# Kernel optimization log

Measured on AMD Instinct MI355X. Metric: run time of the kernel, lower is better.

The kernel has to match this reference:

```python
import jax, jax.numpy as jnp
import numpy as np

N_NODES = 100000
N_EDGES = 1600000
D_IN = 128
D_HID = 128
D_OUT = 128


def setup_inputs() -> dict:
    key = jax.random.key(0)
    ks = jax.random.split(key, 9)
    x = jax.random.normal(ks[0], (N_NODES, D_IN), dtype=jnp.float32)
    src = jax.random.randint(ks[1], (N_EDGES,), 0, N_NODES, dtype=jnp.int32)
    dst = jax.random.randint(ks[2], (N_EDGES,), 0, N_NODES, dtype=jnp.int32)
    def lin(k, fan_in, fan_out):
        bound = 1.0 / np.sqrt(fan_in)
        return jax.random.uniform(k, (fan_out, fan_in), jnp.float32, -bound, bound)
    W_self1 = lin(ks[3], D_IN, D_HID)
    W_neigh1 = lin(ks[4], D_IN, D_HID)
    b1 = jnp.zeros((D_HID,), jnp.float32)
    W_self2 = lin(ks[5], D_HID, D_OUT)
    W_neigh2 = lin(ks[6], D_HID, D_OUT)
    b2 = jnp.zeros((D_OUT,), jnp.float32)
    return {"x": x, "src": src, "dst": dst,
            "W_self1": W_self1, "W_neigh1": W_neigh1, "b1": b1,
            "W_self2": W_self2, "W_neigh2": W_neigh2, "b2": b2}


def _sage_conv(x, src, dst, W_self, W_neigh, b):
    # mean aggregation over in-neighbors (DGL SAGEConv 'mean')
    msg_sum = jax.ops.segment_sum(x[src], dst, num_segments=N_NODES)  # [N, d]
    deg = jax.ops.segment_sum(jnp.ones((src.shape[0],), x.dtype), dst,
                              num_segments=N_NODES)
    h_neigh = msg_sum / jnp.maximum(deg, 1.0)[:, None]
    return x @ W_self.T + h_neigh @ W_neigh.T + b


def reference(x, src, dst, W_self1, W_neigh1, b1, W_self2, W_neigh2, b2):
    h = _sage_conv(x, src, dst, W_self1, W_neigh1, b1)
    h = _sage_conv(h, src, dst, W_self2, W_neigh2, b2)
    # F.normalize(h, p=2, dim=1), eps=1e-12
    norm = jnp.linalg.norm(h, axis=1, keepdims=True)
    return h / jnp.maximum(norm, 1e-12)
```

## Files before the change

### kernel.cpp

```cpp
#include <hip/hip_runtime.h>
#include <math.h>

#define DIM 128
#define CAP 8192
#define BSHIFT 8
#define MAXNB 512

typedef __attribute__((ext_vector_type(8))) short bf16x8;
typedef __attribute__((ext_vector_type(8))) unsigned short us8;
typedef __attribute__((ext_vector_type(4))) float f32x4;

__device__ __forceinline__ unsigned short f2bf_rne(float f) {
    unsigned int u = __float_as_uint(f);
    unsigned int r = (u + 0x7FFFu + ((u >> 16) & 1u)) >> 16;
    return (unsigned short)r;
}
__device__ __forceinline__ float bf2f(unsigned short h) {
    return __uint_as_float(((unsigned int)h) << 16);
}

__global__ void k_zero_int(int* __restrict__ p, int n) {
    int i = blockIdx.x * blockDim.x + threadIdx.x;
    if (i < n) p[i] = 0;
}

__global__ __launch_bounds__(256) void k_xcvt(const float* __restrict__ in,
                                              unsigned short* __restrict__ outb,
                                              int n4) {
    int i = blockIdx.x * 256 + threadIdx.x;
    int stride = gridDim.x * 256;
    for (; i < n4; i += stride) {
        float4 v = *(const float4*)(in + (size_t)i * 4);
        ushort4 o;
        o.x = f2bf_rne(v.x);
        o.y = f2bf_rne(v.y);
        o.z = f2bf_rne(v.z);
        o.w = f2bf_rne(v.w);
        *(ushort4*)(outb + (size_t)i * 4) = o;
    }
}

__global__ __launch_bounds__(256) void k_wcvt(const float* __restrict__ Ws1,
                                              const float* __restrict__ Wn1,
                                              const float* __restrict__ Ws2,
                                              const float* __restrict__ Wn2,
                                              unsigned short* __restrict__ Wh,
                                              unsigned short* __restrict__ Wl) {
    int i = blockIdx.x * 256 + threadIdx.x;
    int l = i >> 15;
    int rem = i & 32767;
    int n = rem >> 8;
    int k = rem & 255;
    const float* W = (k < 128) ? (l ? Ws2 : Ws1) : (l ? Wn2 : Wn1);
    float f = W[n * 128 + (k & 127)];
    unsigned short h = f2bf_rne(f);
    Wh[i] = h;
    Wl[i] = f2bf_rne(f - bf2f(h));
}

__global__ __launch_bounds__(256) void k_bucket(const int* __restrict__ src,
                                                const int* __restrict__ dst,
                                                int* __restrict__ bcur,
                                                unsigned int* __restrict__ tmpe,
                                                int E, int NB, int chunk) {
    __shared__ int hist[MAXNB];
    __shared__ int cur[MAXNB];
    int t = threadIdx.x;
    int begE = blockIdx.x * chunk;
    int endE = begE + chunk;
    if (endE > E) endE = E;

    hist[t] = 0;
    hist[t + 256] = 0;
    __syncthreads();

    for (int e = begE + t; e < endE; e += 256) {
        atomicAdd(&hist[dst[e] >> BSHIFT], 1);
    }
    __syncthreads();

    if (t < NB)  cur[t]  = atomicAdd(&bcur[t], hist[t]);
    int t2 = t + 256;
    if (t2 < NB) cur[t2] = atomicAdd(&bcur[t2], hist[t2]);
    __syncthreads();

    for (int e = begE + t; e < endE; e += 256) {
        int s = src[e];
        int d = dst[e];
        int b = d >> BSHIFT;
        int p = atomicAdd(&cur[b], 1);
        if (p < CAP) tmpe[(size_t)b * CAP + p] = (unsigned int)s | ((unsigned int)(d & 255) << 17);
    }
}

__global__ __launch_bounds__(256) void k_scatter(unsigned int* __restrict__ tmpe,
                                                 const int* __restrict__ bcur,
                                                 int* __restrict__ rs,
                                                 int* __restrict__ cnt,
                                                 int N) {
    __shared__ unsigned int se[CAP];
    __shared__ int hist[256];
    __shared__ int sh[256];
    __shared__ int cur[256];
    int b = blockIdx.x;
    int t = threadIdx.x;
    size_t base = (size_t)b * CAP;
    int m = bcur[b];
    if (m > CAP) m = CAP;
    for (int i = t; i < m; i += 256) se[i] = tmpe[base + i];
    hist[t] = 0;
    __syncthreads();
    for (int i = t; i < m; i += 256) atomicAdd(&hist[se[i] >> 17], 1);
    __syncthreads();
    int v = hist[t];
    sh[t] = v;
    __syncthreads();
    int run = v;
    for (int off = 1; off < 256; off <<= 1) {
        int y = (t >= off) ? sh[t - off] : 0;
        __syncthreads();
        run += y;
        sh[t] = run;
        __syncthreads();
    }
    int excl = run - v;
    int node = (b << BSHIFT) + t;
    if (node < N) {
        rs[node] = (int)base + excl;
        cnt[node] = v;
    }
    cur[t] = excl;
    __syncthreads();
    for (int i = t; i < m; i += 256) {
        unsigned int pk = se[i];
        int d = pk >> 17;
        int p = atomicAdd(&cur[d], 1);
        tmpe[base + p] = pk & 0x1FFFFu;
    }
}

__global__ __launch_bounds__(256) void k_agg(const unsigned short* __restrict__ in,
                                             const int* __restrict__ rs,
                                             const int* __restrict__ cnt,
                                             const unsigned int* __restrict__ esrc,
                                             float* __restrict__ msg, int N) {
    int w = threadIdx.x >> 6;
    int half = (threadIdx.x >> 5) & 1;
    int l32 = threadIdx.x & 31;
    int node = blockIdx.x * 4 + w;
    if (node >= N) return;
    int beg = rs[node];
    int deg = cnt[node];
    int end = beg + deg;
    int c = l32 * 4;
    float ax = 0.f, ay = 0.f, az = 0.f, aw = 0.f;
    int e = beg + half;
    for (; e + 6 < end; e += 8) {
        int s0 = esrc[e];
        int s1 = esrc[e + 2];
        int s2 = esrc[e + 4];
        int s3 = esrc[e + 6];
        ushort4 u0 = *(const ushort4*)(in + (size_t)s0 * DIM + c);
        ushort4 u1 = *(const ushort4*)(in + (size_t)s1 * DIM + c);
        ushort4 u2 = *(const ushort4*)(in + (size_t)s2 * DIM + c);
        ushort4 u3 = *(const ushort4*)(in + (size_t)s3 * DIM + c);
        ax += (bf2f(u0.x) + bf2f(u1.x)) + (bf2f(u2.x) + bf2f(u3.x));
        ay += (bf2f(u0.y) + bf2f(u1.y)) + (bf2f(u2.y) + bf2f(u3.y));
        az += (bf2f(u0.z) + bf2f(u1.z)) + (bf2f(u2.z) + bf2f(u3.z));
        aw += (bf2f(u0.w) + bf2f(u1.w)) + (bf2f(u2.w) + bf2f(u3.w));
    }
    for (; e + 2 < end; e += 4) {
        int s0 = esrc[e];
        int s1 = esrc[e + 2];
        ushort4 u0 = *(const ushort4*)(in + (size_t)s0 * DIM + c);
        ushort4 u1 = *(const ushort4*)(in + (size_t)s1 * DIM + c);
        ax += bf2f(u0.x) + bf2f(u1.x);
        ay += bf2f(u0.y) + bf2f(u1.y);
        az += bf2f(u0.z) + bf2f(u1.z);
        aw += bf2f(u0.w) + bf2f(u1.w);
    }
    if (e < end) {
        int s0 = esrc[e];
        ushort4 u0 = *(const ushort4*)(in + (size_t)s0 * DIM + c);
        ax += bf2f(u0.x);
        ay += bf2f(u0.y);
        az += bf2f(u0.z);
        aw += bf2f(u0.w);
    }
    ax += __shfl_xor(ax, 32);
    ay += __shfl_xor(ay, 32);
    az += __shfl_xor(az, 32);
    aw += __shfl_xor(aw, 32);
    if (half == 0) {
        float invd = 1.0f / fmaxf((float)deg, 1.0f);
        float4 o;
        o.x = ax * invd;
        o.y = ay * invd;
        o.z = az * invd;
        o.w = aw * invd;
        *(float4*)(msg + (size_t)node * DIM + c) = o;
    }
}

template <bool FUSE_NORM>
__global__ __launch_bounds__(256) void k_gemm(const float* __restrict__ A,
                                              const float* __restrict__ Hn,
                                              const unsigned short* __restrict__ Wh,
                                              const unsigned short* __restrict__ Wl,
                                              const float* __restrict__ bias,
                                              float* __restrict__ out,
                                              unsigned short* __restrict__ outb,
                                              int N, int layer) {
    __shared__ __align__(16) unsigned short Ah[128 * 64];
    __shared__ __align__(16) unsigned short Al[128 * 64];
    __shared__ __align__(16) unsigned short Bh[128 * 64];
    __shared__ __align__(16) unsigned short Bl[128 * 64];
    int tid = threadIdx.x;
    int w = tid >> 6;
    int lane = tid & 63;
    int l4 = lane & 15;
    int g = lane >> 4;
    int m0 = blockIdx.x * 128;
    const unsigned short* WhL = Wh + layer * 128 * 256;
    const unsigned short* WlL = Wl + layer * 128 * 256;

    f32x4 acc[2][8];
#pragma unroll
    for (int rt = 0; rt < 2; ++rt)
#pragma unroll
        for (int ct = 0; ct < 8; ++ct) acc[rt][ct] = (f32x4){0.f, 0.f, 0.f, 0.f};

    for (int kb = 0; kb < 256; kb += 64) {
        const float* srcA = (kb < 128) ? A : Hn;
        int ka = kb & 127;
#pragma unroll
        for (int i = 0; i < 4; ++i) {
            int seg = tid + i * 256;
            int row = seg >> 3, k8 = seg & 7;
            int m = m0 + row;
            float4 v0 = make_float4(0.f, 0.f, 0.f, 0.f);
            float4 v1 = make_float4(0.f, 0.f, 0.f, 0.f);
            if (m < N) {
                const float* p = srcA + (size_t)m * DIM + ka + k8 * 8;
                v0 = *(const float4*)p;
                v1 = *(const float4*)(p + 4);
            }
            float f[8] = {v0.x, v0.y, v0.z, v0.w, v1.x, v1.y, v1.z, v1.w};
            us8 hv, lv;
#pragma unroll
            for (int j = 0; j < 8; ++j) {
                unsigned short h = f2bf_rne(f[j]);
                hv[j] = h;
                lv[j] = f2bf_rne(f[j] - bf2f(h));
            }
            int us = row * 64 + ((k8 ^ (row & 7)) << 3);
            *(us8*)&Ah[us] = hv;
            *(us8*)&Al[us] = lv;
        }
#pragma unroll
        for (int i = 0; i < 4; ++i) {
            int seg = tid + i * 256;
            int n = seg >> 3, k8 = seg & 7;
            int gi = n * 256 + kb + k8 * 8;
            us8 hv = *(const us8*)&WhL[gi];
            us8 lv = *(const us8*)&WlL[gi];
            int us = n * 64 + ((k8 ^ (n & 7)) << 3);
            *(us8*)&Bh[us] = hv;
            *(us8*)&Bl[us] = lv;
        }
        __syncthreads();
#pragma unroll
        for (int ks = 0; ks < 2; ++ks) {
            bf16x8 ah[2], al[2];
#pragma unroll
            for (int rt = 0; rt < 2; ++rt) {
                int row = w * 32 + rt * 16 + l4;
                int us = row * 64 + (((ks * 4 + g) ^ (row & 7)) << 3);
                ah[rt] = *(const bf16x8*)&Ah[us];
                al[rt] = *(const bf16x8*)&Al[us];
            }
#pragma unroll
            for (int ct = 0; ct < 8; ++ct) {
                int n = ct * 16 + l4;
                int us = n * 64 + (((ks * 4 + g) ^ (n & 7)) << 3);
                bf16x8 bh = *(const bf16x8*)&Bh[us];
                bf16x8 bl = *(const bf16x8*)&Bl[us];
#pragma unroll
                for (int rt = 0; rt < 2; ++rt) {
                    acc[rt][ct] = __builtin_amdgcn_mfma_f32_16x16x32_bf16(ah[rt], bh, acc[rt][ct], 0, 0, 0);
                    acc[rt][ct] = __builtin_amdgcn_mfma_f32_16x16x32_bf16(ah[rt], bl, acc[rt][ct], 0, 0, 0);
                    acc[rt][ct] = __builtin_amdgcn_mfma_f32_16x16x32_bf16(al[rt], bh, acc[rt][ct], 0, 0, 0);
                }
            }
        }
        __syncthreads();
    }

    float bv[8];
#pragma unroll
    for (int ct = 0; ct < 8; ++ct) bv[ct] = bias[ct * 16 + l4];
#pragma unroll
    for (int rt = 0; rt < 2; ++rt) {
        int rbase = m0 + w * 32 + rt * 16 + g * 4;
        float vals[8][4];
#pragma unroll
        for (int ct = 0; ct < 8; ++ct)
#pragma unroll
            for (int r = 0; r < 4; ++r) vals[ct][r] = acc[rt][ct][r] + bv[ct];
        if (FUSE_NORM) {
            float ss[4];
#pragma unroll
            for (int r = 0; r < 4; ++r) {
                float s = 0.f;
#pragma unroll
                for (int ct = 0; ct < 8; ++ct) s += vals[ct][r] * vals[ct][r];
                s += __shfl_xor(s, 1);
                s += __shfl_xor(s, 2);
                s += __shfl_xor(s, 4);
                s += __shfl_xor(s, 8);
                ss[r] = s;
            }
#pragma unroll
            for (int r = 0; r < 4; ++r) {
                float sc = 1.0f / fmaxf(sqrtf(ss[r]), 1e-12f);
#pragma unroll
                for (int ct = 0; ct < 8; ++ct) vals[ct][r] *= sc;
            }
        }
#pragma unroll
        for (int r = 0; r < 4; ++r) {
            int m = rbase + r;
            if (m < N) {
#pragma unroll
                for (int ct = 0; ct < 8; ++ct) {
                    out[(size_t)m * DIM + ct * 16 + l4] = vals[ct][r];
                    if (!FUSE_NORM)
                        outb[(size_t)m * DIM + ct * 16 + l4] = f2bf_rne(vals[ct][r]);
                }
            }
        }
    }
}

extern "C" void kernel_launch(void* const* d_in, const int* in_sizes, int n_in,
                              void* d_out, int out_size, void* d_ws, size_t ws_size,
                              hipStream_t stream) {
    const float* x   = (const float*)d_in[0];
    const int*   src = (const int*)d_in[1];
    const int*   dst = (const int*)d_in[2];
    const float* Ws1 = (const float*)d_in[3];
    const float* Wn1 = (const float*)d_in[4];
    const float* b1  = (const float*)d_in[5];
    const float* Ws2 = (const float*)d_in[6];
    const float* Wn2 = (const float*)d_in[7];
    const float* b2  = (const float*)d_in[8];
    float* out = (float*)d_out;

    int N = in_sizes[0] / DIM;
    int E = in_sizes[1];
    int NB = (N + (1 << BSHIFT) - 1) >> BSHIFT;

    char* p = (char*)d_ws;
    size_t off = 0;
    auto carve = [&](size_t bytes) {
        void* r = p + off;
        off = (off + bytes + 255) & ~(size_t)255;
        return r;
    };
    unsigned int* tmpe = (unsigned int*)carve((size_t)NB * CAP * 4);
    int* bcur = (int*)carve((size_t)NB * 4);
    int* rs   = (int*)carve((size_t)N * 4);
    int* cnt  = (int*)carve((size_t)N * 4);
    float* msg = (float*)carve((size_t)N * DIM * 4);
    float* h1  = (float*)carve((size_t)N * DIM * 4);
    unsigned short* xb  = (unsigned short*)carve((size_t)N * DIM * 2);
    unsigned short* h1b = (unsigned short*)carve((size_t)N * DIM * 2);
    unsigned short* Wh = (unsigned short*)carve((size_t)2 * 128 * 256 * 2);
    unsigned short* Wl = (unsigned short*)carve((size_t)2 * 128 * 256 * 2);

    k_wcvt<<<256, 256, 0, stream>>>(Ws1, Wn1, Ws2, Wn2, Wh, Wl);
    k_xcvt<<<2048, 256, 0, stream>>>(x, xb, N * DIM / 4);

    int grid_b = 256;
    int chunk = (E + grid_b - 1) / grid_b;
    k_zero_int<<<(NB + 255) / 256, 256, 0, stream>>>(bcur, NB);
    k_bucket<<<grid_b, 256, 0, stream>>>(src, dst, bcur, tmpe, E, NB, chunk);
    k_scatter<<<NB, 256, 0, stream>>>(tmpe, bcur, rs, cnt, N);

    k_agg<<<(N + 3) / 4, 256, 0, stream>>>(xb, rs, cnt, tmpe, msg, N);
    k_gemm<false><<<(N + 127) / 128, 256, 0, stream>>>(x, msg, Wh, Wl, b1, h1, h1b, N, 0);

    k_agg<<<(N + 3) / 4, 256, 0, stream>>>(h1b, rs, cnt, tmpe, msg, N);
    k_gemm<true><<<(N + 127) / 128, 256, 0, stream>>>(h1, msg, Wh, Wl, b2, out, nullptr, N, 1);
}
```

Baseline: 384.4 us.

## Fuse neighbor aggregation into GEMM kernel, keeping mean messages in LDS

```diff
diff --git a/kernel.cpp b/kernel.cpp
--- a/kernel.cpp
+++ b/kernel.cpp
@@ -139,129 +139,132 @@
     }
 }
 
-__global__ __launch_bounds__(256) void k_agg(const unsigned short* __restrict__ in,
-                                             const int* __restrict__ rs,
-                                             const int* __restrict__ cnt,
-                                             const unsigned int* __restrict__ esrc,
-                                             float* __restrict__ msg, int N) {
-    int w = threadIdx.x >> 6;
-    int half = (threadIdx.x >> 5) & 1;
-    int l32 = threadIdx.x & 31;
-    int node = blockIdx.x * 4 + w;
-    if (node >= N) return;
-    int beg = rs[node];
-    int deg = cnt[node];
-    int end = beg + deg;
-    int c = l32 * 4;
-    float ax = 0.f, ay = 0.f, az = 0.f, aw = 0.f;
-    int e = beg + half;
-    for (; e + 6 < end; e += 8) {
-        int s0 = esrc[e];
-        int s1 = esrc[e + 2];
-        int s2 = esrc[e + 4];
-        int s3 = esrc[e + 6];
-        ushort4 u0 = *(const ushort4*)(in + (size_t)s0 * DIM + c);
-        ushort4 u1 = *(const ushort4*)(in + (size_t)s1 * DIM + c);
-        ushort4 u2 = *(const ushort4*)(in + (size_t)s2 * DIM + c);
-        ushort4 u3 = *(const ushort4*)(in + (size_t)s3 * DIM + c);
-        ax += (bf2f(u0.x) + bf2f(u1.x)) + (bf2f(u2.x) + bf2f(u3.x));
-        ay += (bf2f(u0.y) + bf2f(u1.y)) + (bf2f(u2.y) + bf2f(u3.y));
-        az += (bf2f(u0.z) + bf2f(u1.z)) + (bf2f(u2.z) + bf2f(u3.z));
-        aw += (bf2f(u0.w) + bf2f(u1.w)) + (bf2f(u2.w) + bf2f(u3.w));
-    }
-    for (; e + 2 < end; e += 4) {
-        int s0 = esrc[e];
-        int s1 = esrc[e + 2];
-        ushort4 u0 = *(const ushort4*)(in + (size_t)s0 * DIM + c);
-        ushort4 u1 = *(const ushort4*)(in + (size_t)s1 * DIM + c);
-        ax += bf2f(u0.x) + bf2f(u1.x);
-        ay += bf2f(u0.y) + bf2f(u1.y);
-        az += bf2f(u0.z) + bf2f(u1.z);
-        aw += bf2f(u0.w) + bf2f(u1.w);
-    }
-    if (e < end) {
-        int s0 = esrc[e];
-        ushort4 u0 = *(const ushort4*)(in + (size_t)s0 * DIM + c);
-        ax += bf2f(u0.x);
-        ay += bf2f(u0.y);
-        az += bf2f(u0.z);
-        aw += bf2f(u0.w);
-    }
-    ax += __shfl_xor(ax, 32);
-    ay += __shfl_xor(ay, 32);
-    az += __shfl_xor(az, 32);
-    aw += __shfl_xor(aw, 32);
-    if (half == 0) {
-        float invd = 1.0f / fmaxf((float)deg, 1.0f);
-        float4 o;
-        o.x = ax * invd;
-        o.y = ay * invd;
-        o.z = az * invd;
-        o.w = aw * invd;
-        *(float4*)(msg + (size_t)node * DIM + c) = o;
-    }
-}
-
 template <bool FUSE_NORM>
-__global__ __launch_bounds__(256) void k_gemm(const float* __restrict__ A,
-                                              const float* __restrict__ Hn,
-                                              const unsigned short* __restrict__ Wh,
-                                              const unsigned short* __restrict__ Wl,
-                                              const float* __restrict__ bias,
-                                              float* __restrict__ out,
-                                              unsigned short* __restrict__ outb,
-                                              int N, int layer) {
-    __shared__ __align__(16) unsigned short Ah[128 * 64];
-    __shared__ __align__(16) unsigned short Al[128 * 64];
+__global__ __launch_bounds__(256) void k_fused(const float* __restrict__ Afp,
+                                               const unsigned short* __restrict__ Ab,
+                                               const int* __restrict__ rs,
+                                               const int* __restrict__ cnt,
+                                               const unsigned int* __restrict__ esrc,
+                                               const unsigned short* __restrict__ Wh,
+                                               const unsigned short* __restrict__ Wl,
+                                               const float* __restrict__ bias,
+                                               float* __restrict__ out,
+                                               unsigned short* __restrict__ outb,
+                                               int N, int layer) {
+    __shared__ __align__(16) unsigned short Mh[2 * 64 * 64];
+    __shared__ __align__(16) unsigned short Ml[2 * 64 * 64];
+    __shared__ __align__(16) unsigned short Ah[64 * 64];
+    __shared__ __align__(16) unsigned short Al[64 * 64];
     __shared__ __align__(16) unsigned short Bh[128 * 64];
     __shared__ __align__(16) unsigned short Bl[128 * 64];
     int tid = threadIdx.x;
     int w = tid >> 6;
     int lane = tid & 63;
+    int half = lane >> 5;
+    int l32 = lane & 31;
     int l4 = lane & 15;
     int g = lane >> 4;
-    int m0 = blockIdx.x * 128;
+    int m0 = blockIdx.x * 64;
     const unsigned short* WhL = Wh + layer * 128 * 256;
     const unsigned short* WlL = Wl + layer * 128 * 256;
 
-    f32x4 acc[2][8];
-#pragma unroll
-    for (int rt = 0; rt < 2; ++rt)
-#pragma unroll
-        for (int ct = 0; ct < 8; ++ct) acc[rt][ct] = (f32x4){0.f, 0.f, 0.f, 0.f};
-
-    for (int kb = 0; kb < 256; kb += 64) {
-        const float* srcA = (kb < 128) ? A : Hn;
-        int ka = kb & 127;
-#pragma unroll
-        for (int i = 0; i < 4; ++i) {
-            int seg = tid + i * 256;
-            int row = seg >> 3, k8 = seg & 7;
-            int m = m0 + row;
-            float4 v0 = make_float4(0.f, 0.f, 0.f, 0.f);
-            float4 v1 = make_float4(0.f, 0.f, 0.f, 0.f);
-            if (m < N) {
-                const float* p = srcA + (size_t)m * DIM + ka + k8 * 8;
-                v0 = *(const float4*)p;
-                v1 = *(const float4*)(p + 4);
+    int c = l32 * 4;
+    for (int i = 0; i < 16; ++i) {
+        int row = w * 16 + i;
+        int node = m0 + row;
+        int beg = 0, deg = 0;
+        if (node < N) { beg = rs[node]; deg = cnt[node]; }
+        int end = beg + deg;
+        float ax = 0.f, ay = 0.f, az = 0.f, aw_ = 0.f;
+        int e = beg + half;
+        for (; e + 6 < end; e += 8) {
+            int s0 = esrc[e];
+            int s1 = esrc[e + 2];
+            int s2 = esrc[e + 4];
+            int s3 = esrc[e + 6];
+            ushort4 u0 = *(const ushort4*)(Ab + (size_t)s0 * DIM + c);
+            ushort4 u1 = *(const ushort4*)(Ab + (size_t)s1 * DIM + c);
+            ushort4 u2 = *(const ushort4*)(Ab + (size_t)s2 * DIM + c);
+            ushort4 u3 = *(const ushort4*)(Ab + (size_t)s3 * DIM + c);
+            ax += (bf2f(u0.x) + bf2f(u1.x)) + (bf2f(u2.x) + bf2f(u3.x));
+            ay += (bf2f(u0.y) + bf2f(u1.y)) + (bf2f(u2.y) + bf2f(u3.y));
+            az += (bf2f(u0.z) + bf2f(u1.z)) + (bf2f(u2.z) + bf2f(u3.z));
+            aw_ += (bf2f(u0.w) + bf2f(u1.w)) + (bf2f(u2.w) + bf2f(u3.w));
+        }
+        for (; e + 2 < end; e += 4) {
+            int s0 = esrc[e];
+            int s1 = esrc[e + 2];
+            ushort4 u0 = *(const ushort4*)(Ab + (size_t)s0 * DIM + c);
+            ushort4 u1 = *(const ushort4*)(Ab + (size_t)s1 * DIM + c);
+            ax += bf2f(u0.x) + bf2f(u1.x);
+            ay += bf2f(u0.y) + bf2f(u1.y);
+            az += bf2f(u0.z) + bf2f(u1.z);
+            aw_ += bf2f(u0.w) + bf2f(u1.w);
+        }
+        if (e < end) {
+            int s0 = esrc[e];
+            ushort4 u0 = *(const ushort4*)(Ab + (size_t)s0 * DIM + c);
+            ax += bf2f(u0.x);
+            ay += bf2f(u0.y);
+            az += bf2f(u0.z);
+            aw_ += bf2f(u0.w);
+        }
+        ax += __shfl_xor(ax, 32);
+        ay += __shfl_xor(ay, 32);
+        az += __shfl_xor(az, 32);
+        aw_ += __shfl_xor(aw_, 32);
+        if (half == 0) {
+            float invd = 1.0f / fmaxf((float)deg, 1.0f);
+            float f0 = ax * invd, f1 = ay * invd, f2 = az * invd, f3 = aw_ * invd;
+            ushort4 hv, lv;
+            hv.x = f2bf_rne(f0); lv.x = f2bf_rne(f0 - bf2f(hv.x));
+            hv.y = f2bf_rne(f1); lv.y = f2bf_rne(f1 - bf2f(hv.y));
+            hv.z = f2bf_rne(f2); lv.z = f2bf_rne(f2 - bf2f(hv.z));
+            hv.w = f2bf_rne(f3); lv.w = f2bf_rne(f3 - bf2f(hv.w));
+            int ch = l32 >> 4;
+            int k8 = (l32 >> 1) & 7;
+            int us = ch * 4096 + row * 64 + ((k8 ^ (row & 7)) << 3) + ((l32 & 1) << 2);
+            *(ushort4*)&Mh[us] = hv;
+            *(ushort4*)&Ml[us] = lv;
+        }
+    }
+
+    f32x4 acc[8];
+#pragma unroll
+    for (int ct = 0; ct < 8; ++ct) acc[ct] = (f32x4){0.f, 0.f, 0.f, 0.f};
+
+    for (int chunk = 0; chunk < 4; ++chunk) {
+        if (chunk < 2) {
+#pragma unroll
+            for (int i = 0; i < 2; ++i) {
+                int seg = tid + i * 256;
+                int row = seg >> 3, k8 = seg & 7;
+                int m = m0 + row;
+                float4 v0 = make_float4(0.f, 0.f, 0.f, 0.f);
+                float4 v1 = make_float4(0.f, 0.f, 0.f, 0.f);
+                if (m < N) {
+                    const float* p = Afp + (size_t)m * DIM + chunk * 64 + k8 * 8;
+                    v0 = *(const float4*)p;
+                    v1 = *(const float4*)(p + 4);
+                }
+                float f[8] = {v0.x, v0.y, v0.z, v0.w, v1.x, v1.y, v1.z, v1.w};
+                us8 hv, lv;
+#pragma unroll
+                for (int j = 0; j < 8; ++j) {
+                    unsigned short h = f2bf_rne(f[j]);
+                    hv[j] = h;
+                    lv[j] = f2bf_rne(f[j] - bf2f(h));
+                }
+                int us = row * 64 + ((k8 ^ (row & 7)) << 3);
+                *(us8*)&Ah[us] = hv;
+                *(us8*)&Al[us] = lv;
             }
-            float f[8] = {v0.x, v0.y, v0.z, v0.w, v1.x, v1.y, v1.z, v1.w};
-            us8 hv, lv;
-#pragma unroll
-            for (int j = 0; j < 8; ++j) {
-                unsigned short h = f2bf_rne(f[j]);
-                hv[j] = h;
-                lv[j] = f2bf_rne(f[j] - bf2f(h));
-            }
-            int us = row * 64 + ((k8 ^ (row & 7)) << 3);
-            *(us8*)&Ah[us] = hv;
-            *(us8*)&Al[us] = lv;
         }
 #pragma unroll
         for (int i = 0; i < 4; ++i) {
             int seg = tid + i * 256;
             int n = seg >> 3, k8 = seg & 7;
-            int gi = n * 256 + kb + k8 * 8;
+            int gi = n * 256 + chunk * 64 + k8 * 8;
             us8 hv = *(const us8*)&WhL[gi];
             us8 lv = *(const us8*)&WlL[gi];
             int us = n * 64 + ((k8 ^ (n & 7)) << 3);
@@ -269,28 +272,29 @@
             *(us8*)&Bl[us] = lv;
         }
         __syncthreads();
+        int arow = w * 16 + l4;
 #pragma unroll
         for (int ks = 0; ks < 2; ++ks) {
-            bf16x8 ah[2], al[2];
-#pragma unroll
-            for (int rt = 0; rt < 2; ++rt) {
-                int row = w * 32 + rt * 16 + l4;
-                int us = row * 64 + (((ks * 4 + g) ^ (row & 7)) << 3);
-                ah[rt] = *(const bf16x8*)&Ah[us];
-                al[rt] = *(const bf16x8*)&Al[us];
+            int kidx = ks * 4 + g;
+            bf16x8 ah, al;
+            if (chunk < 2) {
+                int us = arow * 64 + ((kidx ^ (arow & 7)) << 3);
+                ah = *(const bf16x8*)&Ah[us];
+                al = *(const bf16x8*)&Al[us];
+            } else {
+                int us = (chunk - 2) * 4096 + arow * 64 + ((kidx ^ (arow & 7)) << 3);
+                ah = *(const bf16x8*)&Mh[us];
+                al = *(const bf16x8*)&Ml[us];
             }
 #pragma unroll
             for (int ct = 0; ct < 8; ++ct) {
                 int n = ct * 16 + l4;
-                int us = n * 64 + (((ks * 4 + g) ^ (n & 7)) << 3);
+                int us = n * 64 + ((kidx ^ (n & 7)) << 3);
                 bf16x8 bh = *(const bf16x8*)&Bh[us];
                 bf16x8 bl = *(const bf16x8*)&Bl[us];
-#pragma unroll
-                for (int rt = 0; rt < 2; ++rt) {
-                    acc[rt][ct] = __builtin_amdgcn_mfma_f32_16x16x32_bf16(ah[rt], bh, acc[rt][ct], 0, 0, 0);
-                    acc[rt][ct] = __builtin_amdgcn_mfma_f32_16x16x32_bf16(ah[rt], bl, acc[rt][ct], 0, 0, 0);
-                    acc[rt][ct] = __builtin_amdgcn_mfma_f32_16x16x32_bf16(al[rt], bh, acc[rt][ct], 0, 0, 0);
-                }
+                acc[ct] = __builtin_amdgcn_mfma_f32_16x16x32_bf16(ah, bh, acc[ct], 0, 0, 0);
+                acc[ct] = __builtin_amdgcn_mfma_f32_16x16x32_bf16(ah, bl, acc[ct], 0, 0, 0);
+                acc[ct] = __builtin_amdgcn_mfma_f32_16x16x32_bf16(al, bh, acc[ct], 0, 0, 0);
             }
         }
         __syncthreads();
@@ -299,44 +303,41 @@
     float bv[8];
 #pragma unroll
     for (int ct = 0; ct < 8; ++ct) bv[ct] = bias[ct * 16 + l4];
-#pragma unroll
-    for (int rt = 0; rt < 2; ++rt) {
-        int rbase = m0 + w * 32 + rt * 16 + g * 4;
-        float vals[8][4];
-#pragma unroll
-        for (int ct = 0; ct < 8; ++ct)
-#pragma unroll
-            for (int r = 0; r < 4; ++r) vals[ct][r] = acc[rt][ct][r] + bv[ct];
-        if (FUSE_NORM) {
-            float ss[4];
-#pragma unroll
-            for (int r = 0; r < 4; ++r) {
-                float s = 0.f;
-#pragma unroll
-                for (int ct = 0; ct < 8; ++ct) s += vals[ct][r] * vals[ct][r];
-                s += __shfl_xor(s, 1);
-                s += __shfl_xor(s, 2);
-                s += __shfl_xor(s, 4);
-                s += __shfl_xor(s, 8);
-                ss[r] = s;
-            }
-#pragma unroll
-            for (int r = 0; r < 4; ++r) {
-                float sc = 1.0f / fmaxf(sqrtf(ss[r]), 1e-12f);
-#pragma unroll
-                for (int ct = 0; ct < 8; ++ct) vals[ct][r] *= sc;
-            }
-        }
+    float vals[8][4];
+#pragma unroll
+    for (int ct = 0; ct < 8; ++ct)
+#pragma unroll
+        for (int r = 0; r < 4; ++r) vals[ct][r] = acc[ct][r] + bv[ct];
+    if (FUSE_NORM) {
+        float ss[4];
 #pragma unroll
         for (int r = 0; r < 4; ++r) {
-            int m = rbase + r;
-            if (m < N) {
-#pragma unroll
-                for (int ct = 0; ct < 8; ++ct) {
-                    out[(size_t)m * DIM + ct * 16 + l4] = vals[ct][r];
-                    if (!FUSE_NORM)
-                        outb[(size_t)m * DIM + ct * 16 + l4] = f2bf_rne(vals[ct][r]);
-                }
+            float s = 0.f;
+#pragma unroll
+            for (int ct = 0; ct < 8; ++ct) s += vals[ct][r] * vals[ct][r];
+            s += __shfl_xor(s, 1);
+            s += __shfl_xor(s, 2);
+            s += __shfl_xor(s, 4);
+            s += __shfl_xor(s, 8);
+            ss[r] = s;
+        }
+#pragma unroll
+        for (int r = 0; r < 4; ++r) {
+            float sc = 1.0f / fmaxf(sqrtf(ss[r]), 1e-12f);
+#pragma unroll
+            for (int ct = 0; ct < 8; ++ct) vals[ct][r] *= sc;
+        }
+    }
+    int rbase = m0 + w * 16 + g * 4;
+#pragma unroll
+    for (int r = 0; r < 4; ++r) {
+        int m = rbase + r;
+        if (m < N) {
+#pragma unroll
+            for (int ct = 0; ct < 8; ++ct) {
+                out[(size_t)m * DIM + ct * 16 + l4] = vals[ct][r];
+                if (outb)
+                    outb[(size_t)m * DIM + ct * 16 + l4] = f2bf_rne(vals[ct][r]);
             }
         }
     }
@@ -371,7 +372,6 @@
     int* bcur = (int*)carve((size_t)NB * 4);
     int* rs   = (int*)carve((size_t)N * 4);
     int* cnt  = (int*)carve((size_t)N * 4);
-    float* msg = (float*)carve((size_t)N * DIM * 4);
     float* h1  = (float*)carve((size_t)N * DIM * 4);
     unsigned short* xb  = (unsigned short*)carve((size_t)N * DIM * 2);
     unsigned short* h1b = (unsigned short*)carve((size_t)N * DIM * 2);
@@ -387,9 +387,8 @@
     k_bucket<<<grid_b, 256, 0, stream>>>(src, dst, bcur, tmpe, E, NB, chunk);
     k_scatter<<<NB, 256, 0, stream>>>(tmpe, bcur, rs, cnt, N);
 
-    k_agg<<<(N + 3) / 4, 256, 0, stream>>>(xb, rs, cnt, tmpe, msg, N);
-    k_gemm<false><<<(N + 127) / 128, 256, 0, stream>>>(x, msg, Wh, Wl, b1, h1, h1b, N, 0);
-
-    k_agg<<<(N + 3) / 4, 256, 0, stream>>>(h1b, rs, cnt, tmpe, msg, N);
-    k_gemm<true><<<(N + 127) / 128, 256, 0, stream>>>(h1, msg, Wh, Wl, b2, out, nullptr, N, 1);
-}
+    int grid_f = (N + 63) / 64;
+    k_fused<false><<<grid_f, 256, 0, stream>>>(x, xb, rs, cnt, tmpe, Wh, Wl, b1, h1, h1b, N, 0);
+
+    k_fused<true><<<grid_f, 256, 0, stream>>>(h1, h1b, rs, cnt, tmpe, Wh, Wl, b2, out, nullptr, N, 1);
+}
```

Measured after the change: 606.7 us. 1.58x slower.
